# Optimization experiments

Hardware: AMD Instinct MI355X
Metric: run time of the kernel (lower is better)

## Reference

```python
import jax, jax.numpy as jnp
import numpy as np

N_NODES = 50000
N_EDGES = 800000
C_IN = 128
C_OUT = 128


def setup_inputs() -> dict:
    key = jax.random.key(0)
    k1, k2, k3, k4 = jax.random.split(key, 4)
    x = jax.random.normal(k1, (N_NODES, C_IN), dtype=jnp.float32)
    edge_index = jax.random.randint(k2, (2, N_EDGES), 0, N_NODES, dtype=jnp.int64)
    # Linear(in, out): weight [out, in], bias [out]
    W = jax.random.normal(k3, (C_OUT, C_IN), dtype=jnp.float32) * (1.0 / np.sqrt(C_IN))
    b = jax.random.normal(k4, (C_OUT,), dtype=jnp.float32) * 0.01
    return {"x": x, "edge_index": edge_index, "W": W, "b": b}


def reference(x, edge_index, W, b):
    # GCN layer: out = D^{-1/2} (A + I) D^{-1/2} x W^T + b
    # Implemented as sparse gather/segment-sum (same math as the dense
    # adjacency matmul in the original, without the O(N^2) blowup).
    n = x.shape[0]
    loops = jnp.arange(n, dtype=edge_index.dtype)
    row = jnp.concatenate([edge_index[0], loops])  # [E+N]
    col = jnp.concatenate([edge_index[1], loops])  # [E+N]
    # degree over col index (as in pyg_utils.degree(edge_index[1], ...))
    ones = jnp.ones(row.shape[0], dtype=x.dtype)
    deg = jax.ops.segment_sum(ones, col, num_segments=n)
    deg_inv_sqrt = jnp.where(deg > 0, jax.lax.rsqrt(deg), 0.0).astype(x.dtype)
    norm = deg_inv_sqrt[row] * deg_inv_sqrt[col]  # [E+N]
    # aggregate: out[i] = sum_{(i,j) in edges} norm * x[j]
    msgs = x[col] * norm[:, None]  # [E+N, C_in]
    agg = jax.ops.segment_sum(msgs, row, num_segments=n)  # [N, C_in]
    return agg @ W.T + b
```

## Files before the change

### kernel.cpp

```cpp
#include <hip/hip_runtime.h>
#include <hip/hip_bf16.h>
#include <hip/hip_fp16.h>

#define C 128
#define NCH 16384
#define CN 4
#define CNODES (CN * NCH)
#define BE 64

typedef _Float16 f16x8 __attribute__((ext_vector_type(8)));
typedef _Float16 f16x4 __attribute__((ext_vector_type(4)));
typedef float f32x4 __attribute__((ext_vector_type(4)));

__global__ __launch_bounds__(256) void k_histgemm(
        const int* __restrict__ row, const int* __restrict__ col,
        unsigned char* __restrict__ part_row, unsigned char* __restrict__ part_col,
        unsigned short* __restrict__ tag, int E, int GB,
        const float* __restrict__ A, const float* __restrict__ W,
        __half* __restrict__ Y16, int n) {
    __shared__ char lds[128 * 256];
    int bid = blockIdx.x;
    int tid = threadIdx.x;

    if (bid >= GB) {
        unsigned* lh = (unsigned*)lds;
        int lb = bid - GB;
        int side = (lb >= CN * BE) ? 1 : 0;
        if (side) lb -= CN * BE;
        int c = lb >> 6;
        int b = lb & (BE - 1);
        for (int i = tid; i < NCH / 4; i += 256) lh[i] = 0u;
        __syncthreads();
        int EPB = (E + BE - 1) / BE;
        int base = b * EPB;
        int end = min(base + EPB, E);
        const int* src = side ? col : row;

#define PROC_ROW(rv, ev)                                                  \
    if (((unsigned)(rv) >> 14) == (unsigned)c) {                          \
        int loc = (rv) & (NCH - 1);                                       \
        unsigned sh = ((unsigned)loc & 3u) << 3;                          \
        unsigned old = atomicAdd(&lh[loc >> 2], 1u << sh);                \
        tag[ev] = (unsigned short)((old >> sh) & 0xffu);                  \
    }
#define PROC_COL(rv)                                                      \
    if (((unsigned)(rv) >> 14) == (unsigned)c) {                          \
        int loc = (rv) & (NCH - 1);                                       \
        atomicAdd(&lh[loc >> 2], 1u << (((unsigned)loc & 3u) << 3));      \
    }
        int nv = 0;
        if ((((uintptr_t)(src + base)) & 15) == 0) nv = (end - base) >> 2;
        const int4* src4 = (const int4*)(src + base);
        if (!side) {
            for (int it = tid; it < nv; it += 256) {
                int4 v = src4[it];
                int e0 = base + it * 4;
                PROC_ROW(v.x, e0);
                PROC_ROW(v.y, e0 + 1);
                PROC_ROW(v.z, e0 + 2);
                PROC_ROW(v.w, e0 + 3);
            }
            for (int e = base + nv * 4 + tid; e < end; e += 256) {
                int r = src[e];
                PROC_ROW(r, e);
            }
        } else {
            for (int it = tid; it < nv; it += 256) {
                int4 v = src4[it];
                PROC_COL(v.x);
                PROC_COL(v.y);
                PROC_COL(v.z);
                PROC_COL(v.w);
            }
            for (int e = base + nv * 4 + tid; e < end; e += 256) {
                int r = src[e];
                PROC_COL(r);
            }
        }
#undef PROC_ROW
#undef PROC_COL
        __syncthreads();
        unsigned* dst = (unsigned*)((side ? part_col : part_row) + (size_t)b * CNODES + c * NCH);
        for (int i = tid; i < NCH / 4; i += 256) dst[i] = lh[i];
        return;
    }

    int w = tid >> 6, lane = tid & 63;
    int m0 = bid * 128;

#pragma unroll
    for (int i = 0; i < 16; ++i) {
        int fidx = i * 256 + tid;
        int nr = fidx >> 5;
        int c4 = fidx & 31;
        float4 wv = *(const float4*)(W + (size_t)nr * C + c4 * 4);
        f16x4 hh = {(_Float16)wv.x, (_Float16)wv.y, (_Float16)wv.z, (_Float16)wv.w};
        unsigned byte = (unsigned)(nr * 256 + c4 * 8);
        byte ^= (unsigned)((nr & 7) << 4);
        *(f16x4*)(lds + byte) = hh;
    }
    __syncthreads();

    int rbase = m0 + w * 32;
    int q = lane >> 4, rl = lane & 15;
    f32x4 acc[2][8] = {};
#pragma unroll
    for (int kc = 0; kc < 4; ++kc) {
        f16x8 af[2];
#pragma unroll
        for (int mt = 0; mt < 2; ++mt) {
            int r = rbase + mt * 16 + rl;
            float4 x0 = make_float4(0.f, 0.f, 0.f, 0.f), x1 = x0;
            if (r < n) {
                const float* srcx = A + (size_t)r * C + kc * 32 + q * 8;
                x0 = *(const float4*)srcx;
                x1 = *(const float4*)(srcx + 4);
            }
            af[mt][0] = (_Float16)x0.x;
            af[mt][1] = (_Float16)x0.y;
            af[mt][2] = (_Float16)x0.z;
            af[mt][3] = (_Float16)x0.w;
            af[mt][4] = (_Float16)x1.x;
            af[mt][5] = (_Float16)x1.y;
            af[mt][6] = (_Float16)x1.z;
            af[mt][7] = (_Float16)x1.w;
        }
#pragma unroll
        for (int nt = 0; nt < 8; ++nt) {
            int nrow = nt * 16 + rl;
            unsigned byte = (unsigned)(nrow * 256 + kc * 64 + q * 16);
            byte ^= (unsigned)((nrow & 7) << 4);
            f16x8 bf = *(f16x8*)(lds + byte);
            acc[0][nt] = __builtin_amdgcn_mfma_f32_16x16x32_f16(af[0], bf, acc[0][nt], 0, 0, 0);
            acc[1][nt] = __builtin_amdgcn_mfma_f32_16x16x32_f16(af[1], bf, acc[1][nt], 0, 0, 0);
        }
    }
    __syncthreads();

#pragma unroll
    for (int mt = 0; mt < 2; ++mt)
#pragma unroll
        for (int nt = 0; nt < 8; ++nt)
#pragma unroll
            for (int i = 0; i < 4; ++i) {
                int row_l = w * 32 + mt * 16 + q * 4 + i;
                int colh = nt * 16 + rl;
                unsigned byte = (unsigned)(row_l * 256 + colh * 2);
                byte ^= (unsigned)((row_l & 7) << 4);
                *(_Float16*)(lds + byte) = (_Float16)acc[mt][nt][i];
            }
    __syncthreads();

#pragma unroll
    for (int it = 0; it < 8; ++it) {
        int idx = it * 256 + tid;
        int row_l = idx >> 4, c8 = idx & 15;
        unsigned byte = (unsigned)(row_l * 256 + c8 * 16);
        byte ^= (unsigned)((row_l & 7) << 4);
        uint4 v = *(uint4*)(lds + byte);
        int gr = m0 + row_l;
        if (gr < n) *(uint4*)(Y16 + (size_t)gr * C + c8 * 8) = v;
    }
}

__global__ __launch_bounds__(256) void k_reduce_scan(
        unsigned char* __restrict__ part_row, const unsigned char* __restrict__ part_col,
        unsigned* __restrict__ start, unsigned* __restrict__ bsum,
        float* __restrict__ dis, int n) {
    __shared__ unsigned s[256];
    int t = threadIdx.x;
    int i = blockIdx.x * 256 + t;
    unsigned acc = 0;
    if (i < n) {
#pragma unroll 8
        for (int b = 0; b < BE; ++b) {
            size_t off = (size_t)b * CNODES + i;
            unsigned v = part_row[off];
            part_row[off] = (unsigned char)acc;
            acc += v;
        }
        unsigned d = 0;
#pragma unroll 8
        for (int b = 0; b < BE; ++b) d += part_col[(size_t)b * CNODES + i];
        dis[i] = rsqrtf((float)(d + 1u));
    }
    unsigned v = acc;
    s[t] = v;
    __syncthreads();
    for (int off = 1; off < 256; off <<= 1) {
        unsigned add = (t >= off) ? s[t - off] : 0u;
        __syncthreads();
        s[t] += add;
        __syncthreads();
    }
    if (i < n) start[i] = s[t] - v;
    if (t == 255) bsum[blockIdx.x] = s[t];
}

__global__ __launch_bounds__(256) void k_scan_final(unsigned* __restrict__ start,
                                                    const unsigned* __restrict__ bsum,
                                                    int n, int E) {
    __shared__ unsigned s[256];
    int t = threadIdx.x;
    int bid = blockIdx.x;
    s[t] = (t < bid) ? bsum[t] : 0u;
    __syncthreads();
    for (int off = 128; off > 0; off >>= 1) {
        if (t < off) s[t] += s[t + off];
        __syncthreads();
    }
    unsigned base = s[0];
    int i = bid * 256 + t;
    if (i < n) start[i] += base;
    if (i == n) start[i] = (unsigned)E;
}

__global__ void k_scatter(const int* __restrict__ row, const int* __restrict__ col,
                          const unsigned short* __restrict__ tag,
                          const unsigned char* __restrict__ boff,
                          const unsigned* __restrict__ start,
                          int* __restrict__ scol, int E, int EPB) {
    int e = blockIdx.x * blockDim.x + threadIdx.x;
    if (e < E) {
        unsigned b = (unsigned)e / (unsigned)EPB;
        int r = row[e];
        unsigned p = start[r] + boff[(size_t)b * CNODES + r] + tag[e];
        scol[p] = col[e];
    }
}

__global__ __launch_bounds__(256) void k_agg(const __half2* __restrict__ Y2,
                                             const int* __restrict__ scol,
                                             const unsigned* __restrict__ start,
                                             const float* __restrict__ dis,
                                             const float* __restrict__ bias,
                                             float* __restrict__ out, int n) {
    int wid = threadIdx.x >> 6;
    int lane = threadIdx.x & 63;
    int r = blockIdx.x * 4 + wid;
    if (r >= n) return;
    unsigned s0 = start[r], s1 = start[r + 1];
    float dr = dis[r];
    float2 self = __half22float2(Y2[(size_t)r * 64 + lane]);
    float2 acc;
    acc.x = dr * self.x;
    acc.y = dr * self.y;
    unsigned k = s0;
    for (; k + 8 <= s1; k += 8) {
        int c[8];
#pragma unroll
        for (int j = 0; j < 8; ++j) c[j] = scol[k + j];
        float d8[8];
#pragma unroll
        for (int j = 0; j < 8; ++j) d8[j] = dis[c[j]];
        __half2 h[8];
#pragma unroll
        for (int j = 0; j < 8; ++j) h[j] = Y2[(size_t)c[j] * 64 + lane];
#pragma unroll
        for (int j = 0; j < 8; ++j) {
            float2 f = __half22float2(h[j]);
            acc.x += d8[j] * f.x;
            acc.y += d8[j] * f.y;
        }
    }
    for (; k < s1; ++k) {
        int cl = scol[k];
        float dc = dis[cl];
        float2 f = __half22float2(Y2[(size_t)cl * 64 + lane]);
        acc.x += dc * f.x;
        acc.y += dc * f.y;
    }
    float2 o;
    o.x = bias[lane * 2 + 0] + dr * acc.x;
    o.y = bias[lane * 2 + 1] + dr * acc.y;
    *(float2*)(out + (size_t)r * C + lane * 2) = o;
}

extern "C" void kernel_launch(void* const* d_in, const int* in_sizes, int n_in,
                              void* d_out, int out_size, void* d_ws, size_t ws_size,
                              hipStream_t stream) {
    const float* x  = (const float*)d_in[0];
    const int*   ei = (const int*)d_in[1];
    const float* W  = (const float*)d_in[2];
    const float* b  = (const float*)d_in[3];
    float* out = (float*)d_out;

    int n = in_sizes[0] / C;
    int E = in_sizes[1] / 2;
    const int* row = ei;
    const int* col = ei + E;

    char* p = (char*)d_ws;
    size_t sz_part = (((size_t)BE * CNODES) + 511) & ~(size_t)511;
    size_t sz_n    = (((size_t)n * 4) + 511) & ~(size_t)511;
    size_t sz_n1   = (((size_t)(n + 1) * 4) + 511) & ~(size_t)511;
    size_t sz_E2   = (((size_t)E * 2) + 511) & ~(size_t)511;
    size_t sz_E4   = (((size_t)E * 4) + 511) & ~(size_t)511;
    size_t off = 0;
    unsigned char*  part_row = (unsigned char*)(p + off);  off += sz_part;
    unsigned char*  part_col = (unsigned char*)(p + off);  off += sz_part;
    unsigned*       start    = (unsigned*)(p + off);       off += sz_n1;
    float*          dis      = (float*)(p + off);          off += sz_n;
    unsigned*       bsum     = (unsigned*)(p + off);       off += 4096;
    unsigned short* tag      = (unsigned short*)(p + off); off += sz_E2;
    int*            scol     = (int*)(p + off);            off += sz_E4;
    __half*         y16      = (__half*)(p + off);

    int NT = 256;
    int NB = (n + NT - 1) / NT;
    int EPB = (E + BE - 1) / BE;
    int GB = (n + 127) / 128;

    k_histgemm<<<GB + 2 * CN * BE, NT, 0, stream>>>(row, col, part_row, part_col,
                                                    tag, E, GB, x, W, y16, n);
    k_reduce_scan<<<NB, NT, 0, stream>>>(part_row, part_col, start, bsum, dis, n);
    k_scan_final<<<NB, NT, 0, stream>>>(start, bsum, n, E);
    k_scatter<<<(E + NT - 1) / NT, NT, 0, stream>>>(row, col, tag, part_row, start, scol, E, EPB);
    k_agg<<<(n + 3) / 4, NT, 0, stream>>>((const __half2*)y16, scol, start, dis, b, out, n);
}
```

Before: 87.90 us.

## Move GEMM after degree scan and pre-scale rows by inverse sqrt degree

The dense transform moves out of the histogram kernel and into the scatter kernel, launched after the degree scan. Each row of x is pre-multiplied by its inverse sqrt degree before the fp16 MFMA. The aggregation kernel then sums plain neighbour rows with no per-edge degree lookup, and uses a wider 16-way unroll with split accumulators. The histogram now uses 2 chunks of 32768 nodes with 8-bit tags, which halves the histogram blocks and tag traffic, at the cost of less overlap between the GEMM and the histogram work.

```diff
diff --git a/kernel.cpp b/kernel.cpp
--- a/kernel.cpp
+++ b/kernel.cpp
@@ -3,8 +3,8 @@
 #include <hip/hip_fp16.h>
 
 #define C 128
-#define NCH 16384
-#define CN 4
+#define NCH 32768
+#define CN 2
 #define CNODES (CN * NCH)
 #define BE 64
 
@@ -12,155 +12,72 @@
 typedef _Float16 f16x4 __attribute__((ext_vector_type(4)));
 typedef float f32x4 __attribute__((ext_vector_type(4)));
 
-__global__ __launch_bounds__(256) void k_histgemm(
+__global__ __launch_bounds__(256) void k_hist(
         const int* __restrict__ row, const int* __restrict__ col,
         unsigned char* __restrict__ part_row, unsigned char* __restrict__ part_col,
-        unsigned short* __restrict__ tag, int E, int GB,
-        const float* __restrict__ A, const float* __restrict__ W,
-        __half* __restrict__ Y16, int n) {
-    __shared__ char lds[128 * 256];
+        unsigned char* __restrict__ tag, int E) {
+    __shared__ unsigned lh[NCH / 4];
     int bid = blockIdx.x;
+    int side = (bid >= CN * BE) ? 1 : 0;
+    int lb = side ? bid - CN * BE : bid;
+    int c = lb >> 6;
+    int b = lb & (BE - 1);
     int tid = threadIdx.x;
-
-    if (bid >= GB) {
-        unsigned* lh = (unsigned*)lds;
-        int lb = bid - GB;
-        int side = (lb >= CN * BE) ? 1 : 0;
-        if (side) lb -= CN * BE;
-        int c = lb >> 6;
-        int b = lb & (BE - 1);
-        for (int i = tid; i < NCH / 4; i += 256) lh[i] = 0u;
-        __syncthreads();
-        int EPB = (E + BE - 1) / BE;
-        int base = b * EPB;
-        int end = min(base + EPB, E);
-        const int* src = side ? col : row;
+    for (int i = tid * 4; i < NCH / 4; i += 1024) {
+        lh[i] = 0u; lh[i + 1] = 0u; lh[i + 2] = 0u; lh[i + 3] = 0u;
+    }
+    __syncthreads();
+    int EPB = (E + BE - 1) / BE;
+    int base = b * EPB;
+    int end = min(base + EPB, E);
+    const int* src = side ? col : row;
 
 #define PROC_ROW(rv, ev)                                                  \
-    if (((unsigned)(rv) >> 14) == (unsigned)c) {                          \
+    if (((unsigned)(rv) >> 15) == (unsigned)c) {                          \
         int loc = (rv) & (NCH - 1);                                       \
         unsigned sh = ((unsigned)loc & 3u) << 3;                          \
         unsigned old = atomicAdd(&lh[loc >> 2], 1u << sh);                \
-        tag[ev] = (unsigned short)((old >> sh) & 0xffu);                  \
+        tag[ev] = (unsigned char)((old >> sh) & 0xffu);                   \
     }
 #define PROC_COL(rv)                                                      \
-    if (((unsigned)(rv) >> 14) == (unsigned)c) {                          \
+    if (((unsigned)(rv) >> 15) == (unsigned)c) {                          \
         int loc = (rv) & (NCH - 1);                                       \
         atomicAdd(&lh[loc >> 2], 1u << (((unsigned)loc & 3u) << 3));      \
     }
-        int nv = 0;
-        if ((((uintptr_t)(src + base)) & 15) == 0) nv = (end - base) >> 2;
-        const int4* src4 = (const int4*)(src + base);
-        if (!side) {
-            for (int it = tid; it < nv; it += 256) {
-                int4 v = src4[it];
-                int e0 = base + it * 4;
-                PROC_ROW(v.x, e0);
-                PROC_ROW(v.y, e0 + 1);
-                PROC_ROW(v.z, e0 + 2);
-                PROC_ROW(v.w, e0 + 3);
-            }
-            for (int e = base + nv * 4 + tid; e < end; e += 256) {
-                int r = src[e];
-                PROC_ROW(r, e);
-            }
-        } else {
-            for (int it = tid; it < nv; it += 256) {
-                int4 v = src4[it];
-                PROC_COL(v.x);
-                PROC_COL(v.y);
-                PROC_COL(v.z);
-                PROC_COL(v.w);
-            }
-            for (int e = base + nv * 4 + tid; e < end; e += 256) {
-                int r = src[e];
-                PROC_COL(r);
-            }
-        }
+    int nv = 0;
+    if ((((uintptr_t)(src + base)) & 15) == 0) nv = (end - base) >> 2;
+    const int4* src4 = (const int4*)(src + base);
+    if (!side) {
+        for (int it = tid; it < nv; it += 256) {
+            int4 v = src4[it];
+            int e0 = base + it * 4;
+            PROC_ROW(v.x, e0);
+            PROC_ROW(v.y, e0 + 1);
+            PROC_ROW(v.z, e0 + 2);
+            PROC_ROW(v.w, e0 + 3);
+        }
+        for (int e = base + nv * 4 + tid; e < end; e += 256) {
+            int r = src[e];
+            PROC_ROW(r, e);
+        }
+    } else {
+        for (int it = tid; it < nv; it += 256) {
+            int4 v = src4[it];
+            PROC_COL(v.x);
+            PROC_COL(v.y);
+            PROC_COL(v.z);
+            PROC_COL(v.w);
+        }
+        for (int e = base + nv * 4 + tid; e < end; e += 256) {
+            int r = src[e];
+            PROC_COL(r);
+        }
+    }
 #undef PROC_ROW
 #undef PROC_COL
-        __syncthreads();
-        unsigned* dst = (unsigned*)((side ? part_col : part_row) + (size_t)b * CNODES + c * NCH);
-        for (int i = tid; i < NCH / 4; i += 256) dst[i] = lh[i];
-        return;
-    }
-
-    int w = tid >> 6, lane = tid & 63;
-    int m0 = bid * 128;
-
-#pragma unroll
-    for (int i = 0; i < 16; ++i) {
-        int fidx = i * 256 + tid;
-        int nr = fidx >> 5;
-        int c4 = fidx & 31;
-        float4 wv = *(const float4*)(W + (size_t)nr * C + c4 * 4);
-        f16x4 hh = {(_Float16)wv.x, (_Float16)wv.y, (_Float16)wv.z, (_Float16)wv.w};
-        unsigned byte = (unsigned)(nr * 256 + c4 * 8);
-        byte ^= (unsigned)((nr & 7) << 4);
-        *(f16x4*)(lds + byte) = hh;
-    }
-    __syncthreads();
-
-    int rbase = m0 + w * 32;
-    int q = lane >> 4, rl = lane & 15;
-    f32x4 acc[2][8] = {};
-#pragma unroll
-    for (int kc = 0; kc < 4; ++kc) {
-        f16x8 af[2];
-#pragma unroll
-        for (int mt = 0; mt < 2; ++mt) {
-            int r = rbase + mt * 16 + rl;
-            float4 x0 = make_float4(0.f, 0.f, 0.f, 0.f), x1 = x0;
-            if (r < n) {
-                const float* srcx = A + (size_t)r * C + kc * 32 + q * 8;
-                x0 = *(const float4*)srcx;
-                x1 = *(const float4*)(srcx + 4);
-            }
-            af[mt][0] = (_Float16)x0.x;
-            af[mt][1] = (_Float16)x0.y;
-            af[mt][2] = (_Float16)x0.z;
-            af[mt][3] = (_Float16)x0.w;
-            af[mt][4] = (_Float16)x1.x;
-            af[mt][5] = (_Float16)x1.y;
-            af[mt][6] = (_Float16)x1.z;
-            af[mt][7] = (_Float16)x1.w;
-        }
-#pragma unroll
-        for (int nt = 0; nt < 8; ++nt) {
-            int nrow = nt * 16 + rl;
-            unsigned byte = (unsigned)(nrow * 256 + kc * 64 + q * 16);
-            byte ^= (unsigned)((nrow & 7) << 4);
-            f16x8 bf = *(f16x8*)(lds + byte);
-            acc[0][nt] = __builtin_amdgcn_mfma_f32_16x16x32_f16(af[0], bf, acc[0][nt], 0, 0, 0);
-            acc[1][nt] = __builtin_amdgcn_mfma_f32_16x16x32_f16(af[1], bf, acc[1][nt], 0, 0, 0);
-        }
-    }
-    __syncthreads();
-
-#pragma unroll
-    for (int mt = 0; mt < 2; ++mt)
-#pragma unroll
-        for (int nt = 0; nt < 8; ++nt)
-#pragma unroll
-            for (int i = 0; i < 4; ++i) {
-                int row_l = w * 32 + mt * 16 + q * 4 + i;
-                int colh = nt * 16 + rl;
-                unsigned byte = (unsigned)(row_l * 256 + colh * 2);
-                byte ^= (unsigned)((row_l & 7) << 4);
-                *(_Float16*)(lds + byte) = (_Float16)acc[mt][nt][i];
-            }
-    __syncthreads();
-
-#pragma unroll
-    for (int it = 0; it < 8; ++it) {
-        int idx = it * 256 + tid;
-        int row_l = idx >> 4, c8 = idx & 15;
-        unsigned byte = (unsigned)(row_l * 256 + c8 * 16);
-        byte ^= (unsigned)((row_l & 7) << 4);
-        uint4 v = *(uint4*)(lds + byte);
-        int gr = m0 + row_l;
-        if (gr < n) *(uint4*)(Y16 + (size_t)gr * C + c8 * 8) = v;
-    }
+    __syncthreads();
+    unsigned* dst = (unsigned*)((side ? part_col : part_row) + (size_t)b * CNODES + c * NCH);
+    for (int i = tid; i < NCH / 4; i += 256) dst[i] = lh[i];
 }
 
 __global__ __launch_bounds__(256) void k_reduce_scan(
@@ -215,21 +132,112 @@
     if (i == n) start[i] = (unsigned)E;
 }
 
-__global__ void k_scatter(const int* __restrict__ row, const int* __restrict__ col,
-                          const unsigned short* __restrict__ tag,
-                          const unsigned char* __restrict__ boff,
-                          const unsigned* __restrict__ start,
-                          int* __restrict__ scol, int E, int EPB) {
-    int e = blockIdx.x * blockDim.x + threadIdx.x;
-    if (e < E) {
-        unsigned b = (unsigned)e / (unsigned)EPB;
-        int r = row[e];
-        unsigned p = start[r] + boff[(size_t)b * CNODES + r] + tag[e];
-        scol[p] = col[e];
-    }
-}
-
-__global__ __launch_bounds__(256) void k_agg(const __half2* __restrict__ Y2,
+__global__ __launch_bounds__(256) void k_scatter_gemm(
+        const int* __restrict__ row, const int* __restrict__ col,
+        const unsigned char* __restrict__ tag, const unsigned char* __restrict__ boff,
+        const unsigned* __restrict__ start, int* __restrict__ scol, int E, int SB,
+        const float* __restrict__ A, const float* __restrict__ W,
+        const float* __restrict__ dis, __half* __restrict__ Z16, int n) {
+    __shared__ char lds[128 * 256];
+    int bid = blockIdx.x;
+    int tid = threadIdx.x;
+    if (bid < SB) {
+        int e = bid * 256 + tid;
+        if (e < E) {
+            int EPB = (E + BE - 1) / BE;
+            unsigned b = (unsigned)e / (unsigned)EPB;
+            int r = row[e];
+            unsigned p = start[r] + boff[(size_t)b * CNODES + r] + tag[e];
+            scol[p] = col[e];
+        }
+        return;
+    }
+    int w = tid >> 6, lane = tid & 63;
+    int m0 = (bid - SB) * 128;
+
+#pragma unroll
+    for (int i = 0; i < 16; ++i) {
+        int fidx = i * 256 + tid;
+        int nr = fidx >> 5;
+        int c4 = fidx & 31;
+        float4 wv = *(const float4*)(W + (size_t)nr * C + c4 * 4);
+        f16x4 hh = {(_Float16)wv.x, (_Float16)wv.y, (_Float16)wv.z, (_Float16)wv.w};
+        unsigned byte = (unsigned)(nr * 256 + c4 * 8);
+        byte ^= (unsigned)((nr & 7) << 4);
+        *(f16x4*)(lds + byte) = hh;
+    }
+    __syncthreads();
+
+    int rbase = m0 + w * 32;
+    int q = lane >> 4, rl = lane & 15;
+    float dm[2];
+#pragma unroll
+    for (int mt = 0; mt < 2; ++mt) {
+        int r = rbase + mt * 16 + rl;
+        dm[mt] = (r < n) ? dis[r] : 0.f;
+    }
+    f32x4 acc[2][8] = {};
+#pragma unroll
+    for (int kc = 0; kc < 4; ++kc) {
+        f16x8 af[2];
+#pragma unroll
+        for (int mt = 0; mt < 2; ++mt) {
+            int r = rbase + mt * 16 + rl;
+            float4 x0 = make_float4(0.f, 0.f, 0.f, 0.f), x1 = x0;
+            if (r < n) {
+                const float* srcx = A + (size_t)r * C + kc * 32 + q * 8;
+                x0 = *(const float4*)srcx;
+                x1 = *(const float4*)(srcx + 4);
+            }
+            float s = dm[mt];
+            af[mt][0] = (_Float16)(x0.x * s);
+            af[mt][1] = (_Float16)(x0.y * s);
+            af[mt][2] = (_Float16)(x0.z * s);
+            af[mt][3] = (_Float16)(x0.w * s);
+            af[mt][4] = (_Float16)(x1.x * s);
+            af[mt][5] = (_Float16)(x1.y * s);
+            af[mt][6] = (_Float16)(x1.z * s);
+            af[mt][7] = (_Float16)(x1.w * s);
+        }
+#pragma unroll
+        for (int nt = 0; nt < 8; ++nt) {
+            int nrow = nt * 16 + rl;
+            unsigned byte = (unsigned)(nrow * 256 + kc * 64 + q * 16);
+            byte ^= (unsigned)((nrow & 7) << 4);
+            f16x8 bf = *(f16x8*)(lds + byte);
+            acc[0][nt] = __builtin_amdgcn_mfma_f32_16x16x32_f16(af[0], bf, acc[0][nt], 0, 0, 0);
+            acc[1][nt] = __builtin_amdgcn_mfma_f32_16x16x32_f16(af[1], bf, acc[1][nt], 0, 0, 0);
+        }
+    }
+    __syncthreads();
+
+#pragma unroll
+    for (int mt = 0; mt < 2; ++mt)
+#pragma unroll
+        for (int nt = 0; nt < 8; ++nt)
+#pragma unroll
+            for (int i = 0; i < 4; ++i) {
+                int row_l = w * 32 + mt * 16 + q * 4 + i;
+                int colh = nt * 16 + rl;
+                unsigned byte = (unsigned)(row_l * 256 + colh * 2);
+                byte ^= (unsigned)((row_l & 7) << 4);
+                *(_Float16*)(lds + byte) = (_Float16)acc[mt][nt][i];
+            }
+    __syncthreads();
+
+#pragma unroll
+    for (int it = 0; it < 8; ++it) {
+        int idx = it * 256 + tid;
+        int row_l = idx >> 4, c8 = idx & 15;
+        unsigned byte = (unsigned)(row_l * 256 + c8 * 16);
+        byte ^= (unsigned)((row_l & 7) << 4);
+        uint4 v = *(uint4*)(lds + byte);
+        int gr = m0 + row_l;
+        if (gr < n) *(uint4*)(Z16 + (size_t)gr * C + c8 * 8) = v;
+    }
+}
+
+__global__ __launch_bounds__(256) void k_agg(const __half2* __restrict__ Z2,
                                              const int* __restrict__ scol,
                                              const unsigned* __restrict__ start,
                                              const float* __restrict__ dis,
@@ -241,38 +249,49 @@
     if (r >= n) return;
     unsigned s0 = start[r], s1 = start[r + 1];
     float dr = dis[r];
-    float2 self = __half22float2(Y2[(size_t)r * 64 + lane]);
-    float2 acc;
-    acc.x = dr * self.x;
-    acc.y = dr * self.y;
+    float2 acc = __half22float2(Z2[(size_t)r * 64 + lane]);
     unsigned k = s0;
-    for (; k + 8 <= s1; k += 8) {
-        int c[8];
-#pragma unroll
-        for (int j = 0; j < 8; ++j) c[j] = scol[k + j];
-        float d8[8];
-#pragma unroll
-        for (int j = 0; j < 8; ++j) d8[j] = dis[c[j]];
-        __half2 h[8];
-#pragma unroll
-        for (int j = 0; j < 8; ++j) h[j] = Y2[(size_t)c[j] * 64 + lane];
-#pragma unroll
-        for (int j = 0; j < 8; ++j) {
+    for (; k + 16 <= s1; k += 16) {
+        int c[16];
+#pragma unroll
+        for (int j = 0; j < 16; ++j) c[j] = scol[k + j];
+        __half2 h[16];
+#pragma unroll
+        for (int j = 0; j < 16; ++j) h[j] = Z2[(size_t)c[j] * 64 + lane];
+        float2 p0 = {0.f, 0.f}, p1 = {0.f, 0.f};
+#pragma unroll
+        for (int j = 0; j < 16; j += 2) {
+            float2 f0 = __half22float2(h[j]);
+            float2 f1 = __half22float2(h[j + 1]);
+            p0.x += f0.x; p0.y += f0.y;
+            p1.x += f1.x; p1.y += f1.y;
+        }
+        acc.x += p0.x + p1.x;
+        acc.y += p0.y + p1.y;
+    }
+    for (; k + 4 <= s1; k += 4) {
+        int c[4];
+#pragma unroll
+        for (int j = 0; j < 4; ++j) c[j] = scol[k + j];
+        __half2 h[4];
+#pragma unroll
+        for (int j = 0; j < 4; ++j) h[j] = Z2[(size_t)c[j] * 64 + lane];
+#pragma unroll
+        for (int j = 0; j < 4; ++j) {
             float2 f = __half22float2(h[j]);
-            acc.x += d8[j] * f.x;
-            acc.y += d8[j] * f.y;
+            acc.x += f.x;
+            acc.y += f.y;
         }
     }
     for (; k < s1; ++k) {
-        int cl = scol[k];
-        float dc = dis[cl];
-        float2 f = __half22float2(Y2[(size_t)cl * 64 + lane]);
-        acc.x += dc * f.x;
-        acc.y += dc * f.y;
-    }
+        float2 f = __half22float2(Z2[(size_t)scol[k] * 64 + lane]);
+        acc.x += f.x;
+        acc.y += f.y;
+    }
+    float2 bv = *(const float2*)(bias + lane * 2);
     float2 o;
-    o.x = bias[lane * 2 + 0] + dr * acc.x;
-    o.y = bias[lane * 2 + 1] + dr * acc.y;
+    o.x = bv.x + dr * acc.x;
+    o.y = bv.y + dr * acc.y;
     *(float2*)(out + (size_t)r * C + lane * 2) = o;
 }
 
@@ -294,7 +313,7 @@
     size_t sz_part = (((size_t)BE * CNODES) + 511) & ~(size_t)511;
     size_t sz_n    = (((size_t)n * 4) + 511) & ~(size_t)511;
     size_t sz_n1   = (((size_t)(n + 1) * 4) + 511) & ~(size_t)511;
-    size_t sz_E2   = (((size_t)E * 2) + 511) & ~(size_t)511;
+    size_t sz_E1   = (((size_t)E) + 511) & ~(size_t)511;
     size_t sz_E4   = (((size_t)E * 4) + 511) & ~(size_t)511;
     size_t off = 0;
     unsigned char*  part_row = (unsigned char*)(p + off);  off += sz_part;
@@ -302,19 +321,19 @@
     unsigned*       start    = (unsigned*)(p + off);       off += sz_n1;
     float*          dis      = (float*)(p + off);          off += sz_n;
     unsigned*       bsum     = (unsigned*)(p + off);       off += 4096;
-    unsigned short* tag      = (unsigned short*)(p + off); off += sz_E2;
+    unsigned char*  tag      = (unsigned char*)(p + off);  off += sz_E1;
     int*            scol     = (int*)(p + off);            off += sz_E4;
-    __half*         y16      = (__half*)(p + off);
+    __half*         z16      = (__half*)(p + off);
 
     int NT = 256;
     int NB = (n + NT - 1) / NT;
-    int EPB = (E + BE - 1) / BE;
+    int SB = (E + NT - 1) / NT;
     int GB = (n + 127) / 128;
 
-    k_histgemm<<<GB + 2 * CN * BE, NT, 0, stream>>>(row, col, part_row, part_col,
-                                                    tag, E, GB, x, W, y16, n);
+    k_hist<<<2 * CN * BE, NT, 0, stream>>>(row, col, part_row, part_col, tag, E);
     k_reduce_scan<<<NB, NT, 0, stream>>>(part_row, part_col, start, bsum, dis, n);
     k_scan_final<<<NB, NT, 0, stream>>>(start, bsum, n, E);
-    k_scatter<<<(E + NT - 1) / NT, NT, 0, stream>>>(row, col, tag, part_row, start, scol, E, EPB);
-    k_agg<<<(n + 3) / 4, NT, 0, stream>>>((const __half2*)y16, scol, start, dis, b, out, n);
-}
+    k_scatter_gemm<<<SB + GB, NT, 0, stream>>>(row, col, tag, part_row, start, scol,
+                                               E, SB, x, W, dis, z16, n);
+    k_agg<<<(n + 3) / 4, NT, 0, stream>>>((const __half2*)z16, scol, start, dis, b, out, n);
+}
```

After: 88.64 us. About the same (+0.8%).
